# Kernel tuning notes

Measured on AMD Instinct MI355X. Metric: run time of the kernel, lower is better.

The kernel has to match this reference:

```python
import jax, jax.numpy as jnp
import numpy as np

TAU = 2.0          # spikingjelly LIFNode default
V_TH = 7.0         # from source
DECREASE = 0.5     # decrease_factor
ALPHA = 4.0        # sigmoid surrogate alpha (spikingjelly default)


@jax.custom_vjp
def spike(v):
    # Heaviside with sigmoid surrogate gradient
    return (v >= 0.0).astype(v.dtype)

def _spike_fwd(v):
    return spike(v), v

def _spike_bwd(v, g):
    s = jax.nn.sigmoid(ALPHA * v)
    return (g * ALPHA * s * (1.0 - s),)

spike.defvjp(_spike_fwd, _spike_bwd)


def setup_inputs() -> dict:
    key = jax.random.key(0)
    k1, k2, k3 = jax.random.split(key, 3)
    B, C, T = 4096, 14, 600
    x = jax.random.normal(k1, (B, C, T), dtype=jnp.float32)
    # weights: normal(mean=0.8, std=0.05) clamped to [0,1]; nn.Linear stores [out,in]
    W1 = jnp.clip(0.8 + 0.05 * jax.random.normal(k2, (14, 14), dtype=jnp.float32), 0.0, 1.0)
    W2 = jnp.clip(0.8 + 0.05 * jax.random.normal(k3, (500, 14), dtype=jnp.float32), 0.0, 1.0)
    return {"x": x, "W1": W1, "W2": W2}


def _forward(x, W1, W2):
    B = x.shape[0]
    xt = jnp.transpose(x, (2, 0, 1))  # [T, B, 14]

    v1_0 = jnp.zeros((B, 14), x.dtype)
    v2_0 = jnp.zeros((B, 500), x.dtype)
    cache0 = jnp.zeros((B, 14), x.dtype)

    def step(carry, x_t):
        v1, v2, cache = carry
        # block 1: linear + decayed feedback of previous spikes
        i1 = x_t @ W1.T + DECREASE * cache
        v1 = v1 + (i1 - v1) / TAU          # LIF charge (decay_input, v_reset=0)
        s1 = spike(v1 - V_TH)
        v1 = v1 * (1.0 - s1)               # hard reset to 0
        # block 2
        i2 = s1 @ W2.T
        v2 = v2 + (i2 - v2) / TAU
        s2 = spike(v2 - V_TH)
        v2 = v2 * (1.0 - s2)
        return (v1, v2, s1), None

    (v1, v2, cache), _ = jax.lax.scan(step, (v1_0, v2_0, cache0), xt)
    return jnp.exp(v2)  # liquid state [B, 500]


def reference(x, W1, W2):
    return _forward(x, W1, W2)
```

## Files before the change

### kernel.cpp

```cpp
#include <hip/hip_runtime.h>
#include <math.h>

#define T      600
#define C      14
#define NOUT   500
#define R      4
#define WW     64
#define DSTR   68
#define NW     6
#define SEG1   268
#define TMID   300
#define CAP    48

__global__ __launch_bounds__(256, 4)
void snn_v4(const float* __restrict__ x, const float* __restrict__ W1,
            const float* __restrict__ W2, float* __restrict__ out) {
    __shared__ float    ds[2 * R * C * DSTR];
    __shared__ unsigned evs[2][R][CAP];
    __shared__ int      ecnt[2][R];

    const int tid = threadIdx.x;
    const int b0  = blockIdx.x * R;
    if (tid < 2 * R) ((int*)ecnt)[tid] = 0;

    const int ss = tid >> 7;
    const int rr = (tid >> 5) & (R - 1);
    const int qq = tid & 31;

    const int wstart = ss ? SEG1 : 0;
    const int tend   = ss ? T    : TMID;
    const int trec   = ss ? TMID : 0;

    const int  cc   = (tid >> 1) & 15;
    const int  ce   = (cc < C) ? cc : (C - 1);
    const bool aact = ((tid & 1) == 0) && (cc < C);

    float2 xv[C];
    {
        const int t0 = wstart + qq * 2;
        #pragma unroll
        for (int j = 0; j < C; ++j)
            xv[j] = *(const float2*)&x[((long)(b0 + rr) * C + j) * T + t0];
    }
    float v1 = 0.f;

    for (int w = 0; w < NW; ++w) {
        const int tw0  = wstart + w * WW;
        const int wlen = (tend - tw0 < WW) ? (tend - tw0) : WW;
        __syncthreads();

        if (wlen > 0) {
            #pragma unroll
            for (int c = 0; c < C; ++c) {
                float ax = 0.f, ay = 0.f;
                #pragma unroll
                for (int j = 0; j < C; ++j) {
                    const float wv = 0.5f * W1[c * C + j];
                    ax = fmaf(xv[j].x, wv, ax);
                    ay = fmaf(xv[j].y, wv, ay);
                }
                *(float2*)&ds[((ss * R + rr) * C + c) * DSTR + qq * 2] =
                    make_float2(ax, ay);
            }
            if (tw0 + WW < tend) {
                const int tn = tw0 + WW + qq * 2;
                if (tn + 1 < T) {
                    #pragma unroll
                    for (int j = 0; j < C; ++j)
                        xv[j] = *(const float2*)&x[((long)(b0 + rr) * C + j) * T + tn];
                }
            }
        }
        __syncthreads();

        if (wlen > 0) {
            const float* dp = &ds[((ss * R + rr) * C + ce) * DSTR];
            for (int q = 0; q < wlen; q += 4) {
                const float4 hd = *(const float4*)&dp[q];
                const float a  = fmaf(v1, 0.5f, hd.x);
                const float b  = fmaf(a,  0.5f, hd.y);
                const float c2 = fmaf(b,  0.5f, hd.z);
                const float d  = fmaf(c2, 0.5f, hd.w);
                const float m  = fmaxf(fmaxf(a, b), fmaxf(c2, d));
                if (__builtin_expect(__ballot(m >= 7.0f) != 0ull, 0)) {
                    float vv = v1;
                    #pragma unroll
                    for (int u = 0; u < 4; ++u) {
                        const float h = (u == 0) ? hd.x : (u == 1) ? hd.y
                                      : (u == 2) ? hd.z : hd.w;
                        vv = fmaf(vv, 0.5f, h);
                        if (vv >= 7.0f) {
                            vv = 0.5f;
                            const int t = tw0 + q + u;
                            if (aact && t >= trec) {
                                const int idx = atomicAdd(&ecnt[ss][rr], 1);
                                if (idx < CAP)
                                    evs[ss][rr][idx] =
                                        ((unsigned)t << 4) | (unsigned)cc;
                            }
                        }
                    }
                    v1 = vv;
                } else {
                    v1 = d;
                }
            }
        }
    }
    __syncthreads();

    const int lane = tid & 31;
    float v2[8];
    #pragma unroll
    for (int k = 0; k < 8; ++k) v2[k] = 0.f;
    int tprev = -1;

    #pragma unroll
    for (int L = 0; L < 2; ++L) {
        const int n = min(ecnt[L][rr], CAP);
        const unsigned* ev = &evs[L][rr][0];
        int e = 0;
        while (e < n) {
            const int t = (int)(ev[e] >> 4);
            float i2[8];
            #pragma unroll
            for (int k = 0; k < 8; ++k) i2[k] = 0.f;
            do {
                const int c = (int)(ev[e] & 15);
                #pragma unroll
                for (int k = 0; k < 8; ++k) {
                    const int o = lane + ((k + 8 * ss) << 5);
                    if (o < NOUT) i2[k] += W2[o * C + c];
                }
                ++e;
            } while (e < n && (int)(ev[e] >> 4) == t);

            const int gap = t - tprev - 1;
            if (gap > 0) {
                #pragma unroll
                for (int k = 0; k < 8; ++k) v2[k] = ldexpf(v2[k], -gap);
            }
            #pragma unroll
            for (int k = 0; k < 8; ++k) {
                const float v = v2[k] + (i2[k] - v2[k]) * 0.5f;
                v2[k] = (v >= 7.0f) ? 0.f : v;
            }
            tprev = t;
        }
    }
    {
        const int gap = (T - 1) - tprev;
        if (gap > 0) {
            #pragma unroll
            for (int k = 0; k < 8; ++k) v2[k] = ldexpf(v2[k], -gap);
        }
    }
    #pragma unroll
    for (int k = 0; k < 8; ++k) {
        const int o = lane + ((k + 8 * ss) << 5);
        if (o < NOUT) out[(long)(b0 + rr) * NOUT + o] = expf(v2[k]);
    }
}

extern "C" void kernel_launch(void* const* d_in, const int* in_sizes, int n_in,
                              void* d_out, int out_size, void* d_ws, size_t ws_size,
                              hipStream_t stream) {
    const float* x  = (const float*)d_in[0];
    const float* W1 = (const float*)d_in[1];
    const float* W2 = (const float*)d_in[2];
    float* o = (float*)d_out;
    const int B = in_sizes[0] / (C * T);
    snn_v4<<<B / R, 256, 0, stream>>>(x, W1, W2, o);
}
```

Before: 53.65 us.

## Use one 64-lane wavefront per batch row with ballot-mask spike events

Replaces the 256-thread block that handled four rows, each split into two overlapping time segments, with one 64-thread block per batch row. That block walks all 600 timesteps in 128-step windows. Spike events are now recorded per timestep as a 14-bit channel mask from a wavefront ballot rather than per-channel atomics. The second layer uses 64 lanes, each covering 8 output neurons. This drops the redundant warm-up overlap and the shared atomics, at the cost of a serial recurrence that is twice as long per block and no prefetch of x across windows.

```diff
diff --git a/kernel.cpp b/kernel.cpp
--- a/kernel.cpp
+++ b/kernel.cpp
@@ -1,55 +1,40 @@
 #include <hip/hip_runtime.h>
 #include <math.h>
 
-#define T      600
-#define C      14
-#define NOUT   500
-#define R      4
-#define WW     64
-#define DSTR   68
-#define NW     6
-#define SEG1   268
-#define TMID   300
-#define CAP    48
+#define T     600
+#define C     14
+#define NOUT  500
+#define W     128
+#define DSTR  132
+#define CAP   64
 
-__global__ __launch_bounds__(256, 4)
-void snn_v4(const float* __restrict__ x, const float* __restrict__ W1,
+__global__ __launch_bounds__(64, 4)
+void snn_v5(const float* __restrict__ x, const float* __restrict__ W1,
             const float* __restrict__ W2, float* __restrict__ out) {
-    __shared__ float    ds[2 * R * C * DSTR];
-    __shared__ unsigned evs[2][R][CAP];
-    __shared__ int      ecnt[2][R];
+    __shared__ float    ds[15 * DSTR];
+    __shared__ unsigned evs[CAP];
+    __shared__ int      ecnt;
 
-    const int tid = threadIdx.x;
-    const int b0  = blockIdx.x * R;
-    if (tid < 2 * R) ((int*)ecnt)[tid] = 0;
+    const int  lane = threadIdx.x;
+    const long row  = blockIdx.x;
+    const float* xr = &x[row * (long)(C * T)];
 
-    const int ss = tid >> 7;
-    const int rr = (tid >> 5) & (R - 1);
-    const int qq = tid & 31;
+    if (lane == 0) ecnt = 0;
+    for (int i = lane; i < DSTR; i += 64) ds[14 * DSTR + i] = 0.f;
 
-    const int wstart = ss ? SEG1 : 0;
-    const int tend   = ss ? T    : TMID;
-    const int trec   = ss ? TMID : 0;
-
-    const int  cc   = (tid >> 1) & 15;
-    const int  ce   = (cc < C) ? cc : (C - 1);
-    const bool aact = ((tid & 1) == 0) && (cc < C);
-
-    float2 xv[C];
-    {
-        const int t0 = wstart + qq * 2;
-        #pragma unroll
-        for (int j = 0; j < C; ++j)
-            xv[j] = *(const float2*)&x[((long)(b0 + rr) * C + j) * T + t0];
-    }
+    const int ce = (lane < C) ? lane : 14;
     float v1 = 0.f;
 
-    for (int w = 0; w < NW; ++w) {
-        const int tw0  = wstart + w * WW;
-        const int wlen = (tend - tw0 < WW) ? (tend - tw0) : WW;
+    for (int t0 = 0; t0 < T; t0 += W) {
+        const int wlen = (T - t0 < W) ? (T - t0) : W;
         __syncthreads();
 
-        if (wlen > 0) {
+        if (2 * lane < wlen) {
+            const int tt = t0 + 2 * lane;
+            float2 xv[C];
+            #pragma unroll
+            for (int j = 0; j < C; ++j)
+                xv[j] = *(const float2*)&xr[j * T + tt];
             #pragma unroll
             for (int c = 0; c < C; ++c) {
                 float ax = 0.f, ay = 0.f;
@@ -59,94 +44,74 @@
                     ax = fmaf(xv[j].x, wv, ax);
                     ay = fmaf(xv[j].y, wv, ay);
                 }
-                *(float2*)&ds[((ss * R + rr) * C + c) * DSTR + qq * 2] =
-                    make_float2(ax, ay);
-            }
-            if (tw0 + WW < tend) {
-                const int tn = tw0 + WW + qq * 2;
-                if (tn + 1 < T) {
-                    #pragma unroll
-                    for (int j = 0; j < C; ++j)
-                        xv[j] = *(const float2*)&x[((long)(b0 + rr) * C + j) * T + tn];
-                }
+                *(float2*)&ds[c * DSTR + 2 * lane] = make_float2(ax, ay);
             }
         }
         __syncthreads();
 
-        if (wlen > 0) {
-            const float* dp = &ds[((ss * R + rr) * C + ce) * DSTR];
-            for (int q = 0; q < wlen; q += 4) {
-                const float4 hd = *(const float4*)&dp[q];
-                const float a  = fmaf(v1, 0.5f, hd.x);
-                const float b  = fmaf(a,  0.5f, hd.y);
-                const float c2 = fmaf(b,  0.5f, hd.z);
-                const float d  = fmaf(c2, 0.5f, hd.w);
-                const float m  = fmaxf(fmaxf(a, b), fmaxf(c2, d));
-                if (__builtin_expect(__ballot(m >= 7.0f) != 0ull, 0)) {
-                    float vv = v1;
-                    #pragma unroll
-                    for (int u = 0; u < 4; ++u) {
-                        const float h = (u == 0) ? hd.x : (u == 1) ? hd.y
-                                      : (u == 2) ? hd.z : hd.w;
-                        vv = fmaf(vv, 0.5f, h);
-                        if (vv >= 7.0f) {
-                            vv = 0.5f;
-                            const int t = tw0 + q + u;
-                            if (aact && t >= trec) {
-                                const int idx = atomicAdd(&ecnt[ss][rr], 1);
-                                if (idx < CAP)
-                                    evs[ss][rr][idx] =
-                                        ((unsigned)t << 4) | (unsigned)cc;
-                            }
-                        }
+        const float* dp = &ds[ce * DSTR];
+        for (int q = 0; q < wlen; q += 4) {
+            const float4 hd = *(const float4*)&dp[q];
+            const float a  = fmaf(v1, 0.5f, hd.x);
+            const float b  = fmaf(a,  0.5f, hd.y);
+            const float c2 = fmaf(b,  0.5f, hd.z);
+            const float d  = fmaf(c2, 0.5f, hd.w);
+            const float m  = fmaxf(fmaxf(a, b), fmaxf(c2, d));
+            if (__builtin_expect(__ballot(m >= 7.0f) != 0ull, 0)) {
+                float vv = v1;
+                #pragma unroll
+                for (int u = 0; u < 4; ++u) {
+                    const float h = (u == 0) ? hd.x : (u == 1) ? hd.y
+                                  : (u == 2) ? hd.z : hd.w;
+                    vv = fmaf(vv, 0.5f, h);
+                    const unsigned mk = (unsigned)__ballot(vv >= 7.0f) & 0x3FFFu;
+                    if (mk) {
+                        if (vv >= 7.0f) vv = 0.5f;
+                        if (lane == 0 && ecnt < CAP)
+                            evs[ecnt++] = ((unsigned)(t0 + q + u) << 14) | mk;
                     }
-                    v1 = vv;
-                } else {
-                    v1 = d;
                 }
+                v1 = vv;
+            } else {
+                v1 = d;
             }
         }
     }
     __syncthreads();
 
-    const int lane = tid & 31;
+    const int n = (ecnt < CAP) ? ecnt : CAP;
     float v2[8];
     #pragma unroll
     for (int k = 0; k < 8; ++k) v2[k] = 0.f;
     int tprev = -1;
 
-    #pragma unroll
-    for (int L = 0; L < 2; ++L) {
-        const int n = min(ecnt[L][rr], CAP);
-        const unsigned* ev = &evs[L][rr][0];
-        int e = 0;
-        while (e < n) {
-            const int t = (int)(ev[e] >> 4);
-            float i2[8];
-            #pragma unroll
-            for (int k = 0; k < 8; ++k) i2[k] = 0.f;
-            do {
-                const int c = (int)(ev[e] & 15);
-                #pragma unroll
-                for (int k = 0; k < 8; ++k) {
-                    const int o = lane + ((k + 8 * ss) << 5);
-                    if (o < NOUT) i2[k] += W2[o * C + c];
-                }
-                ++e;
-            } while (e < n && (int)(ev[e] >> 4) == t);
-
-            const int gap = t - tprev - 1;
-            if (gap > 0) {
-                #pragma unroll
-                for (int k = 0; k < 8; ++k) v2[k] = ldexpf(v2[k], -gap);
-            }
+    for (int e = 0; e < n; ++e) {
+        const unsigned ev = evs[e];
+        const int t = (int)(ev >> 14);
+        unsigned mm = ev & 0x3FFFu;
+        float i2[8];
+        #pragma unroll
+        for (int k = 0; k < 8; ++k) i2[k] = 0.f;
+        while (mm) {
+            const int c = (int)__builtin_ctz(mm);
+            mm &= mm - 1;
             #pragma unroll
             for (int k = 0; k < 8; ++k) {
-                const float v = v2[k] + (i2[k] - v2[k]) * 0.5f;
-                v2[k] = (v >= 7.0f) ? 0.f : v;
+                const int o = lane + (k << 6);
+                if (o < NOUT) i2[k] += W2[o * C + c];
             }
-            tprev = t;
         }
+        const int gap = t - tprev - 1;
+        if (gap > 0) {
+            #pragma unroll
+            for (int k = 0; k < 8; ++k) v2[k] = ldexpf(v2[k], -gap);
+        }
+        #pragma unroll
+        for (int k = 0; k < 8; ++k) {
+            const float v = v2[k] + (i2[k] - v2[k]) * 0.5f;
+            v2[k] = (v >= 7.0f) ? 0.f : v;
+        }
+        tprev = t;
     }
     {
         const int gap = (T - 1) - tprev;
@@ -157,8 +122,8 @@
     }
     #pragma unroll
     for (int k = 0; k < 8; ++k) {
-        const int o = lane + ((k + 8 * ss) << 5);
-        if (o < NOUT) out[(long)(b0 + rr) * NOUT + o] = expf(v2[k]);
+        const int o = lane + (k << 6);
+        if (o < NOUT) out[row * NOUT + o] = expf(v2[k]);
     }
 }
 
@@ -170,5 +135,5 @@
     const float* W2 = (const float*)d_in[2];
     float* o = (float*)d_out;
     const int B = in_sizes[0] / (C * T);
-    snn_v4<<<B / R, 256, 0, stream>>>(x, W1, W2, o);
+    snn_v5<<<B, 64, 0, stream>>>(x, W1, W2, o);
 }
```

Result: faster. 49.15 us (-8.4%).
